# Optimization experiments

Hardware: AMD Instinct MI355X
Metric: run time of the kernel (lower is better)

Reference implementation:

```python
import jax, jax.numpy as jnp
import numpy as np

S_PADDING = 65
T_PADDING = 65


def setup_inputs() -> dict:
    key = jax.random.key(0)
    k1, k2 = jax.random.split(key)
    s = jax.random.normal(k1, (32, 16, 64, 63), dtype=jnp.float32)
    t = jax.random.normal(k2, (32, 16, 64, 63), dtype=jnp.float32)
    return {"s": s, "t": t}


def reference(s, t):
    # s, t: [B, N, L, D] real. Original stacks a zero imaginary part,
    # zero-pads the D dim (dim 3 of the 5D tensor), FFTs along it,
    # then for each shift i rolls fs along N, complex-multiplies with ft,
    # concatenates along N, IFFTs, keeps real part, and permutes to [B, N*N, Dp, L].
    B, N, L, D = s.shape
    s_pad = jnp.pad(s, ((0, 0), (0, 0), (0, 0), (0, S_PADDING)))  # [B,N,L,Dp]
    t_pad = jnp.pad(t, ((0, 0), (0, 0), (0, 0), (0, T_PADDING)))
    FS = jnp.fft.fft(s_pad, axis=-1)  # complex64 [B,N,L,Dp]
    FT = jnp.fft.fft(t_pad, axis=-1)
    # roll(fs, i, axis=1)[:, n] == fs[:, (n - i) % N]; loop i is outer in the cat
    idx = (jnp.arange(N)[None, :] - jnp.arange(N)[:, None]) % N  # [i, n]
    FS_all = FS[:, idx]  # [B, N(i), N(n), L, Dp]
    Hf = FS_all * FT[:, None]  # broadcast over shift dim i
    Dp = D + S_PADDING
    Hf = Hf.reshape(B, N * N, L, Dp)
    H = jnp.fft.ifft(Hf, axis=-1).real  # [B, N*N, L, Dp]
    return H.transpose(0, 1, 3, 2)  # [B, N*N, Dp, L]
```

## Files before the change

kernel.cpp:

```cpp
#include <hip/hip_runtime.h>


#define D_IN 63
#define L_DIM 64
#define N_DIM 16
#define DP 128

__global__ __launch_bounds__(64) void conv_kernel(
    const float* __restrict__ s, const float* __restrict__ t,
    float* __restrict__ out)
{
    const int blk = blockIdx.x;
    const int b  = blk >> 8;
    const int ij = blk & 255;
    const int i  = ij >> 4;
    const int j  = ij & 15;
    const int k  = (j - i) & 15;
    const int l  = threadIdx.x;

    const float* __restrict__ srow = s + ((((size_t)b * N_DIM + k) * L_DIM + l) * D_IN);
    const float* __restrict__ trow = t + ((((size_t)b * N_DIM + j) * L_DIM + l) * D_IN);

    float sv[D_IN], tv[D_IN];
#pragma unroll
    for (int c = 0; c < D_IN; ++c) sv[c] = srow[c];
#pragma unroll
    for (int c = 0; c < D_IN; ++c) tv[c] = trow[c];

    float* __restrict__ orow = out + ((size_t)blk * (DP * L_DIM)) + l;

#pragma unroll
    for (int d0 = 0; d0 < DP; d0 += 16) {
        float acc[16];
#pragma unroll
        for (int dd = 0; dd < 16; ++dd) acc[dd] = 0.0f;

#pragma unroll
        for (int ks = 0; ks < D_IN; ++ks) {
#pragma unroll
            for (int dd = 0; dd < 16; ++dd) {
                const int kt = d0 + dd - ks;
                if (kt >= 0 && kt < D_IN)
                    acc[dd] += sv[ks] * tv[kt];
            }
        }

#pragma unroll
        for (int dd = 0; dd < 16; ++dd)
            orow[(size_t)(d0 + dd) * L_DIM] = acc[dd];
    }
}

extern "C" void kernel_launch(void* const* d_in, const int* in_sizes, int n_in,
                              void* d_out, int out_size, void* d_ws, size_t ws_size,
                              hipStream_t stream) {
    const float* s = (const float*)d_in[0];
    const float* t = (const float*)d_in[1];
    float* out = (float*)d_out;
    hipLaunchKernelGGL(conv_kernel, dim3(32 * N_DIM * N_DIM), dim3(64), 0, stream,
                       s, t, out);
}
```

Baseline: 305.6 us.

## Pre-transpose inputs to D-major layout for coalesced loads in conv kernel

Adds a transpose pass that rewrites s and t into a [B,N,D,L] layout in workspace, so each thread's 63-element row load becomes lane-contiguous across the wavefront instead of strided by 63 floats. Output stores switch to nontemporal stores to avoid polluting cache. The cost is an extra kernel launch and an extra read and write of both inputs, plus dependence on the workspace size. If the workspace is too small, it falls back to the original kernel.

After: 288.9 us. -5.5%, faster.

```diff
diff --git a/kernel.cpp b/kernel.cpp
--- a/kernel.cpp
+++ b/kernel.cpp
@@ -5,8 +5,78 @@
 #define L_DIM 64
 #define N_DIM 16
 #define DP 128
+#define B_DIM 32
 
-__global__ __launch_bounds__(64) void conv_kernel(
+__global__ __launch_bounds__(256) void transpose_kernel(
+    const float* __restrict__ s, const float* __restrict__ t,
+    float* __restrict__ so, float* __restrict__ to)
+{
+    const int tile = blockIdx.x;
+    const int bn   = tile & (B_DIM * N_DIM - 1);
+    const float* __restrict__ src =
+        (tile < B_DIM * N_DIM ? s : t) + (size_t)bn * (L_DIM * D_IN);
+    float* __restrict__ dst =
+        (tile < B_DIM * N_DIM ? so : to) + (size_t)bn * (L_DIM * D_IN);
+
+    __shared__ float lds[L_DIM * D_IN];
+
+    for (int f = threadIdx.x; f < L_DIM * D_IN; f += 256)
+        lds[f] = src[f];
+    __syncthreads();
+
+    for (int g = threadIdx.x; g < L_DIM * D_IN; g += 256) {
+        const int d = g >> 6;
+        const int l = g & 63;
+        dst[g] = lds[l * D_IN + d];
+    }
+}
+
+__global__ __launch_bounds__(64) void conv_kernel_t(
+    const float* __restrict__ st, const float* __restrict__ tt,
+    float* __restrict__ out)
+{
+    const int blk = blockIdx.x;
+    const int b  = blk >> 8;
+    const int ij = blk & 255;
+    const int i  = ij >> 4;
+    const int j  = ij & 15;
+    const int k  = (j - i) & 15;
+    const int l  = threadIdx.x;
+
+    const float* __restrict__ srow = st + (((size_t)b * N_DIM + k) * D_IN) * L_DIM + l;
+    const float* __restrict__ trow = tt + (((size_t)b * N_DIM + j) * D_IN) * L_DIM + l;
+
+    float sv[D_IN], tv[D_IN];
+#pragma unroll
+    for (int c = 0; c < D_IN; ++c) sv[c] = srow[(size_t)c * L_DIM];
+#pragma unroll
+    for (int c = 0; c < D_IN; ++c) tv[c] = trow[(size_t)c * L_DIM];
+
+    float* __restrict__ orow = out + ((size_t)blk * (DP * L_DIM)) + l;
+
+#pragma unroll
+    for (int d0 = 0; d0 < DP; d0 += 16) {
+        float acc[16];
+#pragma unroll
+        for (int dd = 0; dd < 16; ++dd) acc[dd] = 0.0f;
+
+#pragma unroll
+        for (int ks = 0; ks < D_IN; ++ks) {
+#pragma unroll
+            for (int dd = 0; dd < 16; ++dd) {
+                const int kt = d0 + dd - ks;
+                if (kt >= 0 && kt < D_IN)
+                    acc[dd] += sv[ks] * tv[kt];
+            }
+        }
+
+#pragma unroll
+        for (int dd = 0; dd < 16; ++dd)
+            __builtin_nontemporal_store(acc[dd], orow + (size_t)(d0 + dd) * L_DIM);
+    }
+}
+
+__global__ __launch_bounds__(64) void conv_kernel_fallback(
     const float* __restrict__ s, const float* __restrict__ t,
     float* __restrict__ out)
 {
@@ -34,7 +104,6 @@
         float acc[16];
 #pragma unroll
         for (int dd = 0; dd < 16; ++dd) acc[dd] = 0.0f;
-
 #pragma unroll
         for (int ks = 0; ks < D_IN; ++ks) {
 #pragma unroll
@@ -44,7 +113,6 @@
                     acc[dd] += sv[ks] * tv[kt];
             }
         }
-
 #pragma unroll
         for (int dd = 0; dd < 16; ++dd)
             orow[(size_t)(d0 + dd) * L_DIM] = acc[dd];
@@ -57,6 +125,19 @@
     const float* s = (const float*)d_in[0];
     const float* t = (const float*)d_in[1];
     float* out = (float*)d_out;
-    hipLaunchKernelGGL(conv_kernel, dim3(32 * N_DIM * N_DIM), dim3(64), 0, stream,
-                       s, t, out);
+
+    const size_t elems = (size_t)B_DIM * N_DIM * L_DIM * D_IN;
+    const size_t need  = 2 * elems * sizeof(float);
+
+    if (d_ws != nullptr && ws_size >= need) {
+        float* so = (float*)d_ws;
+        float* to = so + elems;
+        hipLaunchKernelGGL(transpose_kernel, dim3(2 * B_DIM * N_DIM), dim3(256), 0, stream,
+                           s, t, so, to);
+        hipLaunchKernelGGL(conv_kernel_t, dim3(B_DIM * N_DIM * N_DIM), dim3(64), 0, stream,
+                           so, to, out);
+    } else {
+        hipLaunchKernelGGL(conv_kernel_fallback, dim3(B_DIM * N_DIM * N_DIM), dim3(64), 0, stream,
+                           s, t, out);
+    }
 }
```
